# Optimization experiments

Measured on AMD Instinct MI355X. Metric: run time of the kernel, lower is better.

The kernel has to match this reference:

```python
import jax, jax.numpy as jnp
import numpy as np

H = 32; D = 128; HID = 4096       # heads, head_dim, hidden
DOFF = 1024; BD = 32; T = DOFF + BD  # prefill tokens, decode batch, total tokens
MAXKV = 513; R = 16; NA = 4       # kv-cache slots, lora rank, num adapters
SCALE = 1.0 / float(np.sqrt(D))


def _add_lora(y, x, wa, wb, segment):
    # segmented (multi-tenant) LoRA: y[t] += x[t] @ A[aid(t)] @ B[aid(t)]
    t = x.shape[0]
    aid = jnp.clip(jnp.searchsorted(segment, jnp.arange(t), side='right') - 1, 0, NA - 1)
    oh = jax.nn.one_hot(aid, NA, dtype=x.dtype)           # [t, NA]
    u = jnp.einsum('th,ahr->atr', x, wa)                  # [NA, t, R]
    v = jnp.einsum('atr,arh->ath', u, wb)                 # [NA, t, HID]
    return y + jnp.einsum('ta,ath->th', oh, v)


def setup_inputs() -> dict:
    key = jax.random.key(0)
    ks = jax.random.split(key, 16)
    f = lambda k, s: (jax.random.normal(k, s, dtype=jnp.float32) * 0.02)
    inp = {
        'hidden_states': f(ks[0], (T, HID)),
        'Wq': f(ks[1], (HID, HID)), 'Wk': f(ks[2], (HID, HID)),
        'Wv': f(ks[3], (HID, HID)), 'Wo': f(ks[4], (HID, HID)),
        'wa_q': f(ks[5], (NA, HID, R)), 'wb_q': f(ks[6], (NA, R, HID)),
        'wa_k': f(ks[7], (NA, HID, R)), 'wb_k': f(ks[8], (NA, R, HID)),
        'wa_v': f(ks[9], (NA, HID, R)), 'wb_v': f(ks[10], (NA, R, HID)),
        'wa_o': f(ks[11], (NA, HID, R)), 'wb_o': f(ks[12], (NA, R, HID)),
        'k_cache': f(ks[13], (BD, MAXKV, H, D)),
        'v_cache': f(ks[14], (BD, MAXKV, H, D)),
        'indptr': jnp.array([0, 200, 456, 800, 1024], dtype=jnp.int32),
        'segment': jnp.array([0, 300, 600, 900, 1056], dtype=jnp.int32),
        'kv_lens': jax.random.randint(ks[15], (BD,), 0, 512, dtype=jnp.int32),
    }
    return inp


def reference(hidden_states, Wq, Wk, Wv, Wo, wa_q, wb_q, wa_k, wb_k, wa_v, wb_v,
              wa_o, wb_o, k_cache, v_cache, indptr, segment, kv_lens):
    # qkv proj + segmented LoRA add
    qp = _add_lora(hidden_states @ Wq, hidden_states, wa_q, wb_q, segment)
    kp = _add_lora(hidden_states @ Wk, hidden_states, wa_k, wb_k, segment)
    vp = _add_lora(hidden_states @ Wv, hidden_states, wa_v, wb_v, segment)

    # ---- ragged prefill attention (causal within each sequence) ----
    q = qp[:DOFF].reshape(DOFF, H, D)
    k = kp[:DOFF].reshape(DOFF, H, D)
    v = vp[:DOFF].reshape(DOFF, H, D)
    idx = jnp.arange(DOFF)
    seg = jnp.searchsorted(indptr, idx, side='right') - 1   # sequence id per token
    m = (seg[:, None] == seg[None, :]) & (idx[None, :] <= idx[:, None])
    s = jnp.einsum('qhd,khd->hqk', q, k) * SCALE
    p = jax.nn.softmax(jnp.where(m[None], s, -1e9), axis=-1)
    out_p = jnp.einsum('hqk,khd->qhd', p, v).reshape(DOFF, HID)

    # ---- paged decode attention (append new kv, attend over cache) ----
    qd = qp[DOFF:].reshape(BD, H, D)
    kd = kp[DOFF:].reshape(BD, H, D)
    vd = vp[DOFF:].reshape(BD, H, D)
    b = jnp.arange(BD)
    kc = k_cache.at[b, kv_lens].set(kd)
    vc = v_cache.at[b, kv_lens].set(vd)
    lens = kv_lens + 1
    md = jnp.arange(MAXKV)[None, :] < lens[:, None]          # [BD, MAXKV]
    sd = jnp.einsum('bhd,bkhd->bhk', qd, kc) * SCALE
    pd = jax.nn.softmax(jnp.where(md[:, None, :], sd, -1e9), axis=-1)
    out_d = jnp.einsum('bhk,bkhd->bhd', pd, vc).reshape(BD, HID)

    attn = jnp.concatenate([out_p, out_d], axis=0)           # [T, HID]
    o = _add_lora(attn @ Wo, attn, wa_o, wb_o, segment)
    return o
```

## Files before the change

kernel.cpp:

```cpp
#include <hip/hip_runtime.h>
#include <hip/hip_bf16.h>

#define H_     32
#define D_     128
#define HID_   4096
#define DOFF_  1024
#define BD_    32
#define T_     1056
#define MAXKV_ 513
#define R_     16
#define NA_    4
#define SCALE_ 0.08838834764831845f

typedef __attribute__((ext_vector_type(8))) short short8;
typedef __attribute__((ext_vector_type(4))) float f32x4;

__device__ __forceinline__ float toF(float x) { return x; }
__device__ __forceinline__ float toF(__hip_bfloat16 x) { return __bfloat162float(x); }
__device__ __forceinline__ void storev(float* p, float v) { *p = v; }
__device__ __forceinline__ void storev(__hip_bfloat16* p, float v) { *p = __float2bfloat16(v); }

__device__ __forceinline__ void gload16(const void* g, void* l) {
  __builtin_amdgcn_global_load_lds(
      (const __attribute__((address_space(1))) unsigned int*)g,
      (__attribute__((address_space(3))) unsigned int*)l, 16, 0, 0);
}

__global__ __launch_bounds__(256) void cast_bf16_kernel(
    const float* __restrict__ X, __hip_bfloat16* __restrict__ Y, int n4) {
  int i = blockIdx.x * 256 + threadIdx.x;
  if (i >= n4) return;
  float4 v = ((const float4*)X)[i];
  __hip_bfloat16 o[4] = {__float2bfloat16(v.x), __float2bfloat16(v.y),
                         __float2bfloat16(v.z), __float2bfloat16(v.w)};
  *(short4*)(Y + (size_t)i * 4) = *(short4*)o;
}

__global__ __launch_bounds__(256) void transpose_cast_kernel(
    const float* __restrict__ W, __hip_bfloat16* __restrict__ WT) {
  __shared__ float tile[32][33];
  int tx = threadIdx.x & 31, ty = threadIdx.x >> 5;
  int r0 = blockIdx.y * 32, c0 = blockIdx.x * 32;
#pragma unroll
  for (int i = 0; i < 32; i += 8)
    tile[ty + i][tx] = W[(size_t)(r0 + ty + i) * HID_ + c0 + tx];
  __syncthreads();
#pragma unroll
  for (int i = 0; i < 32; i += 8)
    WT[(size_t)(c0 + ty + i) * HID_ + r0 + tx] = __float2bfloat16(tile[tx][ty + i]);
}

template <typename XT>
__global__ __launch_bounds__(256) void lora_u_kernel(
    const XT* __restrict__ X, const float* __restrict__ WA,
    const int* __restrict__ segment, float* __restrict__ U) {
  int t = blockIdx.x;
  int tid = threadIdx.x;

  int aid = 0;
#pragma unroll
  for (int i = 1; i < NA_; ++i)
    if (t >= segment[i]) aid = i;

  const XT* x = X + (size_t)t * HID_;
  const float* wa = WA + (size_t)aid * HID_ * R_;

  float part[R_];
#pragma unroll
  for (int r = 0; r < R_; ++r) part[r] = 0.f;

  for (int h = tid; h < HID_; h += 256) {
    float xv = toF(x[h]);
    const float* w = wa + (size_t)h * R_;
#pragma unroll
    for (int r = 0; r < R_; ++r) part[r] += xv * w[r];
  }

  __shared__ float red[256][R_ + 1];
#pragma unroll
  for (int r = 0; r < R_; ++r) red[tid][r] = part[r];
  __syncthreads();
  for (int s = 128; s > 0; s >>= 1) {
    if (tid < s) {
#pragma unroll
      for (int r = 0; r < R_; ++r) red[tid][r] += red[tid + s][r];
    }
    __syncthreads();
  }
  if (tid < R_) U[(size_t)t * R_ + tid] = red[0][tid];
}

template <typename OUT_T>
__global__ __launch_bounds__(256) void gemm_bf16_lora_kernel(
    const __hip_bfloat16* __restrict__ Xb, const __hip_bfloat16* __restrict__ WT,
    const float* __restrict__ U, const float* __restrict__ BMAT,
    const int* __restrict__ segment, OUT_T* __restrict__ Y, int Trows) {
  __shared__ __hip_bfloat16 As[128 * 32];
  __shared__ __hip_bfloat16 Bs[128 * 32];

  const int tid = threadIdx.x;
  const int lane = tid & 63;
  const int wave = tid >> 6;
  const int wr = (wave >> 1) * 64;
  const int wc = (wave & 1) * 64;
  const int m0 = blockIdx.y * 128, n0 = blockIdx.x * 128;

  const int srow = tid >> 2;
  const int sel = (tid & 3) * 8;
  int ar0 = m0 + srow;      if (ar0 >= Trows) ar0 = Trows - 1;
  int ar1 = m0 + srow + 64; if (ar1 >= Trows) ar1 = Trows - 1;
  const __hip_bfloat16* gA0 = Xb + (size_t)ar0 * HID_ + sel;
  const __hip_bfloat16* gA1 = Xb + (size_t)ar1 * HID_ + sel;
  const __hip_bfloat16* gB0 = WT + (size_t)(n0 + srow) * HID_ + sel;
  const __hip_bfloat16* gB1 = WT + (size_t)(n0 + srow + 64) * HID_ + sel;
  __hip_bfloat16* lA = As + tid * 8;
  __hip_bfloat16* lB = Bs + tid * 8;

  const int lrow = lane & 15;
  const int lk = (lane >> 4) * 8;
  const __hip_bfloat16* fA = As + (wr + lrow) * 32 + lk;
  const __hip_bfloat16* fB = Bs + (wc + lrow) * 32 + lk;

  f32x4 acc[4][4] = {};

  for (int k0 = 0; k0 < HID_; k0 += 32) {
    gload16(gA0, lA);
    gload16(gA1, lA + 2048);
    gload16(gB0, lB);
    gload16(gB1, lB + 2048);
    gA0 += 32; gA1 += 32; gB0 += 32; gB1 += 32;
    __syncthreads();
    short8 a[4], b[4];
#pragma unroll
    for (int mi = 0; mi < 4; ++mi) a[mi] = *(const short8*)(fA + mi * 512);
#pragma unroll
    for (int ni = 0; ni < 4; ++ni) b[ni] = *(const short8*)(fB + ni * 512);
#pragma unroll
    for (int mi = 0; mi < 4; ++mi)
#pragma unroll
      for (int ni = 0; ni < 4; ++ni)
        acc[mi][ni] = __builtin_amdgcn_mfma_f32_16x16x32_bf16(a[mi], b[ni], acc[mi][ni], 0, 0, 0);
    __syncthreads();
  }

  const int crow = (lane >> 4) * 4;
  const int ccol = lane & 15;
#pragma unroll
  for (int mi = 0; mi < 4; ++mi) {
    const int tb = m0 + wr + mi * 16 + crow;
#pragma unroll
    for (int i = 0; i < 4; ++i) {
      const int t = tb + i;
      if (t >= Trows) continue;
      int aid = 0;
#pragma unroll
      for (int s = 1; s < NA_; ++s)
        if (t >= segment[s]) aid = s;
      const float* ub = U + (size_t)t * R_;
      const float* bb = BMAT + (size_t)aid * R_ * HID_;
#pragma unroll
      for (int ni = 0; ni < 4; ++ni) {
        const int n = n0 + wc + ni * 16 + ccol;
        float v = acc[mi][ni][i];
        const float* bc = bb + n;
#pragma unroll
        for (int r = 0; r < R_; ++r) v += ub[r] * bc[(size_t)r * HID_];
        storev(Y + (size_t)t * HID_ + n, v);
      }
    }
  }
}

#define QB 64
#define KB 32

__global__ __launch_bounds__(256) void attn_prefill_mfma_kernel(
    const __hip_bfloat16* __restrict__ qp, const __hip_bfloat16* __restrict__ kp,
    const __hip_bfloat16* __restrict__ vp, const int* __restrict__ indptr,
    __hip_bfloat16* __restrict__ attn) {
  __shared__ __hip_bfloat16 Klds[KB * 128];
  __shared__ __hip_bfloat16 Vt[128 * 40];
  __shared__ __hip_bfloat16 Plds[4][16 * 40];

  const int tid = threadIdx.x;
  const int lane = tid & 63;
  const int wave = tid >> 6;
  const int g = lane >> 4;
  const int lc = lane & 15;
  const int q0 = blockIdx.x * QB;
  const int h = blockIdx.y;

  int qrows[4], qstart[4];
#pragma unroll
  for (int i = 0; i < 4; ++i) {
    int q = q0 + wave * 16 + g * 4 + i;
    qrows[i] = q;
    int s0 = 0;
#pragma unroll
    for (int j = 1; j < NA_; ++j)
      if (q >= indptr[j]) s0 = indptr[j];
    qstart[i] = s0;
  }

  short8 aq[4];
  {
    const __hip_bfloat16* qrow = qp + (size_t)(q0 + wave * 16 + lc) * HID_ + h * D_;
#pragma unroll
    for (int dc = 0; dc < 4; ++dc)
      aq[dc] = *(const short8*)(qrow + dc * 32 + g * 8);
  }

  float mrow[4], lrow[4];
#pragma unroll
  for (int i = 0; i < 4; ++i) { mrow[i] = -1e30f; lrow[i] = 0.f; }
  f32x4 o[8] = {};

  int ks0 = 0;
#pragma unroll
  for (int j = 1; j < NA_; ++j)
    if (q0 >= indptr[j]) ks0 = indptr[j];
  const int kt0 = ks0 & ~(KB - 1);

  const int sr = tid >> 4;
  const int sc = tid & 15;

  for (int kt = kt0; kt < q0 + QB; kt += KB) {
    gload16(kp + (size_t)(kt + sr) * HID_ + h * D_ + ((sc ^ (sr & 7)) * 8),
            Klds + tid * 8);
    gload16(kp + (size_t)(kt + 16 + sr) * HID_ + h * D_ + ((sc ^ (sr & 7)) * 8),
            Klds + 2048 + tid * 8);
    {
      short8 v0 = *(const short8*)(vp + (size_t)(kt + sr) * HID_ + h * D_ + sc * 8);
      short8 v1 = *(const short8*)(vp + (size_t)(kt + 16 + sr) * HID_ + h * D_ + sc * 8);
      const __hip_bfloat16* e0 = (const __hip_bfloat16*)&v0;
      const __hip_bfloat16* e1 = (const __hip_bfloat16*)&v1;
#pragma unroll
      for (int e = 0; e < 8; ++e) {
        Vt[(sc * 8 + e) * 40 + sr] = e0[e];
        Vt[(sc * 8 + e) * 40 + sr + 16] = e1[e];
      }
    }
    __syncthreads();

    f32x4 s0v = {}, s1v = {};
#pragma unroll
    for (int dc = 0; dc < 4; ++dc) {
      const int cb = dc * 4 + g;
      short8 bk0 = *(const short8*)(Klds + lc * 128 + ((cb ^ (lc & 7)) * 8));
      short8 bk1 = *(const short8*)(Klds + (16 + lc) * 128 + ((cb ^ (lc & 7)) * 8));
      s0v = __builtin_amdgcn_mfma_f32_16x16x32_bf16(aq[dc], bk0, s0v, 0, 0, 0);
      s1v = __builtin_amdgcn_mfma_f32_16x16x32_bf16(aq[dc], bk1, s1v, 0, 0, 0);
    }

    const int kl0 = kt + lc, kl1 = kt + 16 + lc;
#pragma unroll
    for (int i = 0; i < 4; ++i) {
      float sm0 = s0v[i] * SCALE_;
      float sm1 = s1v[i] * SCALE_;
      bool v0ok = (kl0 >= qstart[i]) && (kl0 <= qrows[i]);
      bool v1ok = (kl1 >= qstart[i]) && (kl1 <= qrows[i]);
      float mx = fmaxf(v0ok ? sm0 : -1e30f, v1ok ? sm1 : -1e30f);
#pragma unroll
      for (int off = 1; off < 16; off <<= 1)
        mx = fmaxf(mx, __shfl_xor(mx, off));
      float mnew = fmaxf(mrow[i], mx);
      float alpha = __expf(mrow[i] - mnew);
      float p0 = v0ok ? __expf(sm0 - mnew) : 0.f;
      float p1 = v1ok ? __expf(sm1 - mnew) : 0.f;
      lrow[i] = lrow[i] * alpha + p0 + p1;
      mrow[i] = mnew;
#pragma unroll
      for (int dc = 0; dc < 8; ++dc) o[dc][i] *= alpha;
      Plds[wave][(g * 4 + i) * 40 + lc] = __float2bfloat16(p0);
      Plds[wave][(g * 4 + i) * 40 + 16 + lc] = __float2bfloat16(p1);
    }

    asm volatile("s_waitcnt lgkmcnt(0)" ::: "memory");

    short8 ap = *(const short8*)(&Plds[wave][lc * 40 + g * 8]);
#pragma unroll
    for (int dc = 0; dc < 8; ++dc) {
      short8 bv = *(const short8*)(&Vt[(dc * 16 + lc) * 40 + g * 8]);
      o[dc] = __builtin_amdgcn_mfma_f32_16x16x32_bf16(ap, bv, o[dc], 0, 0, 0);
    }
    __syncthreads();
  }

#pragma unroll
  for (int i = 0; i < 4; ++i) {
    float l = lrow[i];
#pragma unroll
    for (int off = 1; off < 16; off <<= 1) l += __shfl_xor(l, off);
    lrow[i] = 1.f / l;
  }
#pragma unroll
  for (int dc = 0; dc < 8; ++dc)
#pragma unroll
    for (int i = 0; i < 4; ++i)
      attn[(size_t)qrows[i] * HID_ + h * D_ + dc * 16 + lc] =
          __float2bfloat16(o[dc][i] * lrow[i]);
}

__global__ __launch_bounds__(256) void attn_decode_kernel(
    const __hip_bfloat16* __restrict__ qp, const __hip_bfloat16* __restrict__ kp,
    const __hip_bfloat16* __restrict__ vp, const float* __restrict__ kcache,
    const float* __restrict__ vcache, const int* __restrict__ kv_lens,
    __hip_bfloat16* __restrict__ attn) {
  int h = blockIdx.x;
  int b = blockIdx.y;
  int wave = threadIdx.x >> 6;
  int lane = threadIdx.x & 63;
  int t = DOFF_ + b;

  const __hip_bfloat16* qptr = qp + (size_t)t * HID_ + h * D_;
  float q0 = toF(qptr[lane]), q1 = toF(qptr[lane + 64]);
  int len = kv_lens[b];

  int cnt = len + 1;
  int chunk = (cnt + 3) >> 2;
  int ks = wave * chunk;
  int ke = ks + chunk; if (ke > cnt) ke = cnt;

  float m = -1e30f, l = 0.f, acc0 = 0.f, acc1 = 0.f;
  for (int k = ks; k < ke; ++k) {
    float kv0, kv1, vv0, vv1;
    if (k == len) {
      const __hip_bfloat16* kptr = kp + (size_t)t * HID_ + h * D_;
      const __hip_bfloat16* vptr = vp + (size_t)t * HID_ + h * D_;
      kv0 = toF(kptr[lane]); kv1 = toF(kptr[lane + 64]);
      vv0 = toF(vptr[lane]); vv1 = toF(vptr[lane + 64]);
    } else {
      size_t base = (((size_t)b * MAXKV_ + k) * H_ + h) * D_;
      kv0 = kcache[base + lane]; kv1 = kcache[base + lane + 64];
      vv0 = vcache[base + lane]; vv1 = vcache[base + lane + 64];
    }
    float s = q0 * kv0 + q1 * kv1;
#pragma unroll
    for (int off = 32; off > 0; off >>= 1) s += __shfl_xor(s, off);
    s *= SCALE_;
    float mnew = fmaxf(m, s);
    float alpha = __expf(m - mnew);
    float p = __expf(s - mnew);
    acc0 = acc0 * alpha + p * vv0;
    acc1 = acc1 * alpha + p * vv1;
    l = l * alpha + p;
    m = mnew;
  }

  __shared__ float sm[4], sl[4], sacc[4][128];
  if (lane == 0) { sm[wave] = m; sl[wave] = l; }
  sacc[wave][lane] = acc0;
  sacc[wave][lane + 64] = acc1;
  __syncthreads();
  if (wave == 0) {
    float M = fmaxf(fmaxf(sm[0], sm[1]), fmaxf(sm[2], sm[3]));
    float L = 0.f, A0 = 0.f, A1 = 0.f;
#pragma unroll
    for (int w = 0; w < 4; ++w) {
      float sc = __expf(sm[w] - M);
      L += sl[w] * sc;
      A0 += sacc[w][lane] * sc;
      A1 += sacc[w][lane + 64] * sc;
    }
    float inv = 1.f / L;
    __hip_bfloat16* outp = attn + (size_t)t * HID_ + h * D_;
    storev(outp + lane, A0 * inv);
    storev(outp + lane + 64, A1 * inv);
  }
}

extern "C" void kernel_launch(void* const* d_in, const int* in_sizes, int n_in,
                              void* d_out, int out_size, void* d_ws, size_t ws_size,
                              hipStream_t stream) {
  const float* hidden  = (const float*)d_in[0];
  const float* Wq      = (const float*)d_in[1];
  const float* Wk      = (const float*)d_in[2];
  const float* Wv      = (const float*)d_in[3];
  const float* Wo      = (const float*)d_in[4];
  const float* wa_q    = (const float*)d_in[5];
  const float* wb_q    = (const float*)d_in[6];
  const float* wa_k    = (const float*)d_in[7];
  const float* wb_k    = (const float*)d_in[8];
  const float* wa_v    = (const float*)d_in[9];
  const float* wb_v    = (const float*)d_in[10];
  const float* wa_o    = (const float*)d_in[11];
  const float* wb_o    = (const float*)d_in[12];
  const float* k_cache = (const float*)d_in[13];
  const float* v_cache = (const float*)d_in[14];
  const int*   indptr  = (const int*)d_in[15];
  const int*   segment = (const int*)d_in[16];
  const int*   kv_lens = (const int*)d_in[17];
  float* out = (float*)d_out;

  const size_t PROJ = (size_t)T_ * HID_;
  __hip_bfloat16* Xb    = (__hip_bfloat16*)d_ws;
  __hip_bfloat16* qp    = Xb + PROJ;
  __hip_bfloat16* kp    = qp + PROJ;
  __hip_bfloat16* vp    = kp + PROJ;
  __hip_bfloat16* attnb = vp + PROJ;
  __hip_bfloat16* WT    = attnb + PROJ;
  float* u_q = (float*)(WT + (size_t)HID_ * HID_);
  float* u_k = u_q + (size_t)T_ * R_;
  float* u_v = u_k + (size_t)T_ * R_;
  float* u_o = u_v + (size_t)T_ * R_;

  const int n4 = (int)(PROJ / 4);
  dim3 tg(HID_ / 32, HID_ / 32);
  dim3 gg(HID_ / 128, (T_ + 127) / 128);

  cast_bf16_kernel<<<(n4 + 255) / 256, 256, 0, stream>>>(hidden, Xb, n4);
  lora_u_kernel<float><<<T_, 256, 0, stream>>>(hidden, wa_q, segment, u_q);
  lora_u_kernel<float><<<T_, 256, 0, stream>>>(hidden, wa_k, segment, u_k);
  lora_u_kernel<float><<<T_, 256, 0, stream>>>(hidden, wa_v, segment, u_v);

  transpose_cast_kernel<<<tg, 256, 0, stream>>>(Wq, WT);
  gemm_bf16_lora_kernel<__hip_bfloat16><<<gg, 256, 0, stream>>>(Xb, WT, u_q, wb_q, segment, qp, T_);
  transpose_cast_kernel<<<tg, 256, 0, stream>>>(Wk, WT);
  gemm_bf16_lora_kernel<__hip_bfloat16><<<gg, 256, 0, stream>>>(Xb, WT, u_k, wb_k, segment, kp, T_);
  transpose_cast_kernel<<<tg, 256, 0, stream>>>(Wv, WT);
  gemm_bf16_lora_kernel<__hip_bfloat16><<<gg, 256, 0, stream>>>(Xb, WT, u_v, wb_v, segment, vp, T_);

  attn_prefill_mfma_kernel<<<dim3(DOFF_ / QB, H_), 256, 0, stream>>>(qp, kp, vp, indptr, attnb);
  attn_decode_kernel<<<dim3(H_, BD_), 256, 0, stream>>>(qp, kp, vp, k_cache, v_cache,
                                                        kv_lens, attnb);

  lora_u_kernel<__hip_bfloat16><<<T_, 256, 0, stream>>>(attnb, wa_o, segment, u_o);
  transpose_cast_kernel<<<tg, 256, 0, stream>>>(Wo, WT);
  gemm_bf16_lora_kernel<float><<<gg, 256, 0, stream>>>(attnb, WT, u_o, wb_o, segment, out, T_);
}
```

Baseline: 723.1 us.

## Shrink GEMM M-tile, vectorize transpose, batch LoRA-A projections into one launch

The projection GEMM tile drops from 128x128 to 64x128, which doubles the block count to fill more CUs for T=1056 rows and cuts padding waste in the last row tile. The weight transpose-cast moves to 64x64 tiles with float4 loads and short4 stores. The LoRA down-projection kernel now handles q/k/v in a single 2D launch and loads x four elements at a time. The smaller GEMM tile lowers per-block reuse of the B operand, raising global and LDS traffic per FLOP.

```diff
diff --git a/kernel.cpp b/kernel.cpp
--- a/kernel.cpp
+++ b/kernel.cpp
@@ -26,6 +26,16 @@
       (__attribute__((address_space(3))) unsigned int*)l, 16, 0, 0);
 }
 
+__device__ __forceinline__ void load4(const float* p, float* v) {
+  float4 t = *(const float4*)p;
+  v[0] = t.x; v[1] = t.y; v[2] = t.z; v[3] = t.w;
+}
+__device__ __forceinline__ void load4(const __hip_bfloat16* p, float* v) {
+  short4 t = *(const short4*)p;
+  const __hip_bfloat16* e = (const __hip_bfloat16*)&t;
+  v[0] = toF(e[0]); v[1] = toF(e[1]); v[2] = toF(e[2]); v[3] = toF(e[3]);
+}
+
 __global__ __launch_bounds__(256) void cast_bf16_kernel(
     const float* __restrict__ X, __hip_bfloat16* __restrict__ Y, int n4) {
   int i = blockIdx.x * 256 + threadIdx.x;
@@ -38,24 +48,39 @@
 
 __global__ __launch_bounds__(256) void transpose_cast_kernel(
     const float* __restrict__ W, __hip_bfloat16* __restrict__ WT) {
-  __shared__ float tile[32][33];
-  int tx = threadIdx.x & 31, ty = threadIdx.x >> 5;
-  int r0 = blockIdx.y * 32, c0 = blockIdx.x * 32;
-#pragma unroll
-  for (int i = 0; i < 32; i += 8)
-    tile[ty + i][tx] = W[(size_t)(r0 + ty + i) * HID_ + c0 + tx];
+  __shared__ float tile[64][65];
+  int tx = threadIdx.x & 15;
+  int ty = threadIdx.x >> 4;
+  int r0 = blockIdx.y * 64, c0 = blockIdx.x * 64;
+#pragma unroll
+  for (int s = 0; s < 64; s += 16) {
+    float4 v = *(const float4*)(W + (size_t)(r0 + ty + s) * HID_ + c0 + tx * 4);
+    tile[ty + s][tx * 4 + 0] = v.x;
+    tile[ty + s][tx * 4 + 1] = v.y;
+    tile[ty + s][tx * 4 + 2] = v.z;
+    tile[ty + s][tx * 4 + 3] = v.w;
+  }
   __syncthreads();
 #pragma unroll
-  for (int i = 0; i < 32; i += 8)
-    WT[(size_t)(c0 + ty + i) * HID_ + r0 + tx] = __float2bfloat16(tile[tx][ty + i]);
+  for (int s = 0; s < 64; s += 16) {
+    int c = ty + s;
+    __hip_bfloat16 o[4];
+#pragma unroll
+    for (int e = 0; e < 4; ++e) o[e] = __float2bfloat16(tile[tx * 4 + e][c]);
+    *(short4*)(WT + (size_t)(c0 + c) * HID_ + r0 + tx * 4) = *(short4*)o;
+  }
 }
 
 template <typename XT>
 __global__ __launch_bounds__(256) void lora_u_kernel(
-    const XT* __restrict__ X, const float* __restrict__ WA,
-    const int* __restrict__ segment, float* __restrict__ U) {
+    const XT* __restrict__ X, const float* __restrict__ WA0,
+    const float* __restrict__ WA1, const float* __restrict__ WA2,
+    const int* __restrict__ segment, float* __restrict__ U0,
+    float* __restrict__ U1, float* __restrict__ U2) {
   int t = blockIdx.x;
   int tid = threadIdx.x;
+  const float* WA = blockIdx.y == 0 ? WA0 : (blockIdx.y == 1 ? WA1 : WA2);
+  float* U = blockIdx.y == 0 ? U0 : (blockIdx.y == 1 ? U1 : U2);
 
   int aid = 0;
 #pragma unroll
@@ -69,11 +94,15 @@
 #pragma unroll
   for (int r = 0; r < R_; ++r) part[r] = 0.f;
 
-  for (int h = tid; h < HID_; h += 256) {
-    float xv = toF(x[h]);
-    const float* w = wa + (size_t)h * R_;
-#pragma unroll
-    for (int r = 0; r < R_; ++r) part[r] += xv * w[r];
+  for (int h = tid * 4; h < HID_; h += 1024) {
+    float xv[4];
+    load4(x + h, xv);
+#pragma unroll
+    for (int e = 0; e < 4; ++e) {
+      const float* w = wa + (size_t)(h + e) * R_;
+#pragma unroll
+      for (int r = 0; r < R_; ++r) part[r] += xv[e] * w[r];
+    }
   }
 
   __shared__ float red[256][R_ + 1];
@@ -95,22 +124,20 @@
     const __hip_bfloat16* __restrict__ Xb, const __hip_bfloat16* __restrict__ WT,
     const float* __restrict__ U, const float* __restrict__ BMAT,
     const int* __restrict__ segment, OUT_T* __restrict__ Y, int Trows) {
-  __shared__ __hip_bfloat16 As[128 * 32];
+  __shared__ __hip_bfloat16 As[64 * 32];
   __shared__ __hip_bfloat16 Bs[128 * 32];
 
   const int tid = threadIdx.x;
   const int lane = tid & 63;
   const int wave = tid >> 6;
-  const int wr = (wave >> 1) * 64;
+  const int wr = (wave >> 1) * 32;
   const int wc = (wave & 1) * 64;
-  const int m0 = blockIdx.y * 128, n0 = blockIdx.x * 128;
+  const int m0 = blockIdx.y * 64, n0 = blockIdx.x * 128;
 
   const int srow = tid >> 2;
   const int sel = (tid & 3) * 8;
-  int ar0 = m0 + srow;      if (ar0 >= Trows) ar0 = Trows - 1;
-  int ar1 = m0 + srow + 64; if (ar1 >= Trows) ar1 = Trows - 1;
+  int ar0 = m0 + srow; if (ar0 >= Trows) ar0 = Trows - 1;
   const __hip_bfloat16* gA0 = Xb + (size_t)ar0 * HID_ + sel;
-  const __hip_bfloat16* gA1 = Xb + (size_t)ar1 * HID_ + sel;
   const __hip_bfloat16* gB0 = WT + (size_t)(n0 + srow) * HID_ + sel;
   const __hip_bfloat16* gB1 = WT + (size_t)(n0 + srow + 64) * HID_ + sel;
   __hip_bfloat16* lA = As + tid * 8;
@@ -121,22 +148,21 @@
   const __hip_bfloat16* fA = As + (wr + lrow) * 32 + lk;
   const __hip_bfloat16* fB = Bs + (wc + lrow) * 32 + lk;
 
-  f32x4 acc[4][4] = {};
+  f32x4 acc[2][4] = {};
 
   for (int k0 = 0; k0 < HID_; k0 += 32) {
     gload16(gA0, lA);
-    gload16(gA1, lA + 2048);
     gload16(gB0, lB);
     gload16(gB1, lB + 2048);
-    gA0 += 32; gA1 += 32; gB0 += 32; gB1 += 32;
+    gA0 += 32; gB0 += 32; gB1 += 32;
     __syncthreads();
-    short8 a[4], b[4];
-#pragma unroll
-    for (int mi = 0; mi < 4; ++mi) a[mi] = *(const short8*)(fA + mi * 512);
+    short8 a[2], b[4];
+#pragma unroll
+    for (int mi = 0; mi < 2; ++mi) a[mi] = *(const short8*)(fA + mi * 512);
 #pragma unroll
     for (int ni = 0; ni < 4; ++ni) b[ni] = *(const short8*)(fB + ni * 512);
 #pragma unroll
-    for (int mi = 0; mi < 4; ++mi)
+    for (int mi = 0; mi < 2; ++mi)
 #pragma unroll
       for (int ni = 0; ni < 4; ++ni)
         acc[mi][ni] = __builtin_amdgcn_mfma_f32_16x16x32_bf16(a[mi], b[ni], acc[mi][ni], 0, 0, 0);
@@ -146,7 +172,7 @@
   const int crow = (lane >> 4) * 4;
   const int ccol = lane & 15;
 #pragma unroll
-  for (int mi = 0; mi < 4; ++mi) {
+  for (int mi = 0; mi < 2; ++mi) {
     const int tb = m0 + wr + mi * 16 + crow;
 #pragma unroll
     for (int i = 0; i < 4; ++i) {
@@ -405,13 +431,12 @@
   float* u_o = u_v + (size_t)T_ * R_;
 
   const int n4 = (int)(PROJ / 4);
-  dim3 tg(HID_ / 32, HID_ / 32);
-  dim3 gg(HID_ / 128, (T_ + 127) / 128);
+  dim3 tg(HID_ / 64, HID_ / 64);
+  dim3 gg(HID_ / 128, (T_ + 63) / 64);
 
   cast_bf16_kernel<<<(n4 + 255) / 256, 256, 0, stream>>>(hidden, Xb, n4);
-  lora_u_kernel<float><<<T_, 256, 0, stream>>>(hidden, wa_q, segment, u_q);
-  lora_u_kernel<float><<<T_, 256, 0, stream>>>(hidden, wa_k, segment, u_k);
-  lora_u_kernel<float><<<T_, 256, 0, stream>>>(hidden, wa_v, segment, u_v);
+  lora_u_kernel<float><<<dim3(T_, 3), 256, 0, stream>>>(
+      hidden, wa_q, wa_k, wa_v, segment, u_q, u_k, u_v);
 
   transpose_cast_kernel<<<tg, 256, 0, stream>>>(Wq, WT);
   gemm_bf16_lora_kernel<__hip_bfloat16><<<gg, 256, 0, stream>>>(Xb, WT, u_q, wb_q, segment, qp, T_);
@@ -424,7 +449,8 @@
   attn_decode_kernel<<<dim3(H_, BD_), 256, 0, stream>>>(qp, kp, vp, k_cache, v_cache,
                                                         kv_lens, attnb);
 
-  lora_u_kernel<__hip_bfloat16><<<T_, 256, 0, stream>>>(attnb, wa_o, segment, u_o);
+  lora_u_kernel<__hip_bfloat16><<<dim3(T_, 1), 256, 0, stream>>>(
+      attnb, wa_o, wa_o, wa_o, segment, u_o, u_o, u_o);
   transpose_cast_kernel<<<tg, 256, 0, stream>>>(Wo, WT);
   gemm_bf16_lora_kernel<float><<<gg, 256, 0, stream>>>(attnb, WT, u_o, wb_o, segment, out, T_);
 }
```

New measurement: 777.7 us. 7.6% more time.
